# Performance work log

Hardware: AMD Instinct MI355X
Metric: run time of the kernel (lower is better)

## Reference

```python
import jax, jax.numpy as jnp
import numpy as np

N, M, NNZ, N_C, D = 4096, 4096, 262144, 4, 128
ADD_RATIO, TEMP = 0.1, 0.5


def setup_inputs() -> dict:
    key = jax.random.key(0)
    ks = jax.random.split(key, 6)
    X = jax.random.normal(ks[0], (N, D), dtype=jnp.float32)
    V = jax.random.randint(ks[1], (NNZ,), 0, N)
    E = jax.random.randint(ks[2], (NNZ,), 0, M)
    # incidence matrix consistent with the (V, E) pairs
    H = jnp.zeros((N, M), jnp.float32).at[V, E].set(1.0)
    incident_mask_prob = jax.random.uniform(ks[3], (N, M), jnp.float32, 1e-4, 1.0 - 1e-4)
    cos_weight = jax.random.normal(ks[4], (N_C, D), dtype=jnp.float32)
    eps = jax.random.uniform(ks[5], (N, M), jnp.float32, 1e-6, 1.0 - 1e-6)
    return {"X": X, "H": H, "V": V, "E": E,
            "incident_mask_prob": incident_mask_prob,
            "cos_weight": cos_weight, "eps": eps}


def _l2norm(x):
    # F.normalize(p=2, dim=-1): x / max(||x||, 1e-12)
    return x / jnp.maximum(jnp.linalg.norm(x, axis=-1, keepdims=True), 1e-12)


def reference(X, H, V, E, incident_mask_prob, cos_weight, eps):
    # scatter-mean of node embeddings into edge embeddings: eX [M, D]
    counts = jax.ops.segment_sum(jnp.ones((NNZ,), X.dtype), E, num_segments=M)
    eX = jax.ops.segment_sum(X[V], E, num_segments=M) / jnp.maximum(counts, 1.0)[:, None]

    node_fc = _l2norm(X[:, None, :] * cos_weight[None])   # [N, C, D]
    edge_fc = _l2norm(eX[:, None, :] * cos_weight[None])  # [M, C, D]
    # mean over C of per-channel cosine sims -> S [N, M]
    S = jnp.einsum('ncd,mcd->nm', node_fc, edge_fc) / N_C
    S = S.at[V, E].set(-1e30)  # mask existing incidences

    num_add = max(1, int(ADD_RATIO * NNZ))
    _, idx = jax.lax.top_k(S.reshape(-1), num_add)
    row = idx // M
    col = idx % M
    delta_H = jnp.zeros_like(H).at[row, col].set(1.0)
    enriched_H = H + delta_H

    # gumbel-sigmoid with straight-through estimator
    logit = (jnp.log(eps) - jnp.log(1.0 - eps)
             + jnp.log(incident_mask_prob + 1e-8)
             - jnp.log(1.0 - incident_mask_prob + 1e-8))
    soft = jax.nn.sigmoid(logit / TEMP)
    hard = (soft > 0.5).astype(soft.dtype)
    incident_mask = hard - jax.lax.stop_gradient(soft) + soft
    return enriched_H * incident_mask
```

## Files before the change

### kernel.cpp

```cpp
#include <hip/hip_runtime.h>

#define N_NODES 4096
#define M_EDGES 4096
#define NNZ_K   262144
#define NCH     4
#define DIM     128
#define KDIM    512
#define NM      (N_NODES * M_EDGES)
#define NUM_ADD 26214
#define NCB     2048
#define NFB     32768
#define NSEG    8
#define SEGSTR  16
#define CAPSEG  32768
#define CAPSEG2 16384

#define EXD_OFF   0ull
#define AFC_OFF   4194304ull
#define BFC_OFF   8388608ull
#define BKT_OFF   12582912ull
#define CVAL_OFF  13631488ull
#define CIDX_OFF  15728640ull
#define CNT_OFF   17039360ull
#define OFFS_OFF  17055744ull
#define CUR_OFF   17072132ull
#define HIST_OFF  17088516ull
#define FHIST_OFF 17096708ull
#define SCL_OFF   17227784ull
#define SEGC_OFF  17227848ull
#define ZERO_BYTES (17228872ull - CNT_OFF)
#define NINV_OFF  17228928ull
#define EINV_OFF  17360000ull
#define CIDX2_OFF 17491072ull

typedef short bf16x8 __attribute__((ext_vector_type(8)));
typedef float f32x4  __attribute__((ext_vector_type(4)));

#define GLOAD_LDS16(gsrc, ldst)                                                 \
    __builtin_amdgcn_global_load_lds(                                           \
        (const __attribute__((address_space(1))) void*)(gsrc),                  \
        (__attribute__((address_space(3))) void*)(ldst), 16, 0, 0)

__device__ __forceinline__ int bin_c(float s) {
    int b = (int)floorf((s + 1.0f) * 1024.0f);
    return min(max(b, 0), NCB - 1);
}

__device__ __forceinline__ int fbin_of(double v, int bstar) {
    double lo = (double)(bstar - 12) * (2.0 / 2048.0) - 1.0;
    double wd = (28.0 * (2.0 / 2048.0)) / (double)NFB;
    int f = (int)floor((v - lo) / wd);
    return min(max(f, 0), NFB - 1);
}

__device__ __forceinline__ float hard_mask(float p, float e) {
    float logit = logf(e) - logf(1.0f - e) + logf(p + 1e-8f) - logf(1.0f - p + 1e-8f);
    float soft  = 1.0f / (1.0f + expf(-2.0f * logit));
    return (soft > 0.5f) ? 1.0f : 0.0f;
}

__device__ __forceinline__ unsigned short to_bf16_rtne(float f) {
    unsigned int b = __float_as_uint(f);
    b += 0x7FFFu + ((b >> 16) & 1u);
    return (unsigned short)(b >> 16);
}

__global__ void k_count(const int* __restrict__ E, int* __restrict__ cnt) {
    int k = blockIdx.x * 256 + threadIdx.x;
    if (k < NNZ_K) atomicAdd(&cnt[E[k]], 1);
}

__global__ __launch_bounds__(256) void k_scan(const int* __restrict__ cnt, int* __restrict__ offs) {
    __shared__ int part[256];
    int t = threadIdx.x;
    int loc[16]; int s = 0;
    for (int j = 0; j < 16; ++j) { loc[j] = cnt[t * 16 + j]; s += loc[j]; }
    part[t] = s;
    __syncthreads();
    if (t == 0) { int acc = 0; for (int i = 0; i < 256; ++i) { int v = part[i]; part[i] = acc; acc += v; } }
    __syncthreads();
    int acc = part[t];
    for (int j = 0; j < 16; ++j) { offs[t * 16 + j] = acc; acc += loc[j]; }
    if (t == 255) offs[4096] = acc;
}

__global__ void k_fill(const int* __restrict__ E, const int* __restrict__ offs,
                       int* __restrict__ cur, int* __restrict__ bkt) {
    int k = blockIdx.x * 256 + threadIdx.x;
    if (k < NNZ_K) {
        int e = E[k];
        int pos = atomicAdd(&cur[e], 1);
        bkt[offs[e] + pos] = k;
    }
}

__global__ __launch_bounds__(128) void k_edge_mean(
        const int* __restrict__ Vv, const int* __restrict__ cnt,
        const int* __restrict__ offs, const int* __restrict__ bkt,
        const float* __restrict__ X, double* __restrict__ eXd) {
    __shared__ int sk[1024];
    __shared__ int sv[1024];
    int m = blockIdx.x;
    int c = cnt[m]; if (c > 1024) c = 1024;
    int off = offs[m];
    for (int t = threadIdx.x; t < c; t += 128) sk[t] = bkt[off + t];
    __syncthreads();
    for (int t = threadIdx.x; t < c; t += 128) {
        int key = sk[t]; int r = 0;
        for (int j = 0; j < c; ++j) r += (sk[j] < key);
        sv[r] = Vv[key];
    }
    __syncthreads();
    int d = threadIdx.x;
    double s = 0.0;
    for (int j = 0; j < c; ++j) s += (double)X[sv[j] * DIM + d];
    eXd[m * DIM + d] = s / (double)(c > 1 ? c : 1);
}

template <typename T>
__global__ __launch_bounds__(128) void k_fc(const T* __restrict__ in,
                                            const float* __restrict__ w,
                                            unsigned short* __restrict__ out,
                                            double* __restrict__ dinv) {
    __shared__ double red[128];
    int n = blockIdx.x, d = threadIdx.x;
    double x = (double)in[n * DIM + d];
    for (int c = 0; c < NCH; ++c) {
        double v = x * (double)w[c * DIM + d];
        red[d] = v * v;
        __syncthreads();
        for (int s = 64; s > 0; s >>= 1) { if (d < s) red[d] += red[d + s]; __syncthreads(); }
        double denom = fmax(sqrt(red[0]), 1e-12);
        __syncthreads();
        out[n * KDIM + c * DIM + d] = to_bf16_rtne((float)(v / denom));
        if (d == 0) dinv[n * NCH + c] = 1.0 / denom;
    }
}

__global__ __launch_bounds__(256) void k_gemm_mfma(const unsigned short* __restrict__ A,
                                                   const unsigned short* __restrict__ B,
                                                   float* __restrict__ S) {
    __shared__ short As[128][32];
    __shared__ short Bs[128][32];
    int tid = threadIdx.x;
    int row0 = blockIdx.y * 128, col0 = blockIdx.x * 128;
    int w = tid >> 6, l = tid & 63;
    int wr = (w >> 1) * 64, wc = (w & 1) * 64;
    f32x4 acc[4][4] = {};
    int lrow = l >> 2, lcol = (l & 3) * 8;
    int rb0 = (w * 2 + 0) * 16, rb1 = (w * 2 + 1) * 16;
    const unsigned short* sA0 = A + (size_t)(row0 + rb0 + lrow) * KDIM + lcol;
    const unsigned short* sA1 = A + (size_t)(row0 + rb1 + lrow) * KDIM + lcol;
    const unsigned short* sB0 = B + (size_t)(col0 + rb0 + lrow) * KDIM + lcol;
    const unsigned short* sB1 = B + (size_t)(col0 + rb1 + lrow) * KDIM + lcol;
    for (int k0 = 0; k0 < KDIM; k0 += 32) {
        __syncthreads();
        GLOAD_LDS16(sA0 + k0, &As[rb0][0]);
        GLOAD_LDS16(sA1 + k0, &As[rb1][0]);
        GLOAD_LDS16(sB0 + k0, &Bs[rb0][0]);
        GLOAD_LDS16(sB1 + k0, &Bs[rb1][0]);
        __syncthreads();
        int kq = (l >> 4) * 8;
        bf16x8 af[4], bfr[4];
        #pragma unroll
        for (int m = 0; m < 4; ++m) af[m] = *(const bf16x8*)&As[wr + m * 16 + (l & 15)][kq];
        #pragma unroll
        for (int n = 0; n < 4; ++n) bfr[n] = *(const bf16x8*)&Bs[wc + n * 16 + (l & 15)][kq];
        #pragma unroll
        for (int m = 0; m < 4; ++m)
            #pragma unroll
            for (int n = 0; n < 4; ++n)
                acc[m][n] = __builtin_amdgcn_mfma_f32_16x16x32_bf16(af[m], bfr[n], acc[m][n], 0, 0, 0);
    }
    #pragma unroll
    for (int m = 0; m < 4; ++m) {
        int r = row0 + wr + m * 16 + (l >> 4) * 4;
        #pragma unroll
        for (int n = 0; n < 4; ++n) {
            int c = col0 + wc + n * 16 + (l & 15);
            #pragma unroll
            for (int j = 0; j < 4; ++j)
                S[(size_t)(r + j) * M_EDGES + c] = 0.25f * acc[m][n][j];
        }
    }
}

__global__ void k_mask(const int* __restrict__ Vv, const int* __restrict__ E,
                       float* __restrict__ S) {
    int k = blockIdx.x * 256 + threadIdx.x;
    if (k < NNZ_K) S[(size_t)Vv[k] * M_EDGES + E[k]] = -1e30f;
}

__global__ __launch_bounds__(256) void k_hist_coarse(const float4* __restrict__ S4,
                                                     int* __restrict__ hist) {
    __shared__ int h[4][NCB + 8];
    int t = threadIdx.x;
    for (int i = t; i < 4 * (NCB + 8); i += 256) ((int*)h)[i] = 0;
    __syncthreads();
    int* hc = h[t & 3];
    int stride = gridDim.x * 256;
    for (int i = blockIdx.x * 256 + t; i < NM / 4; i += stride) {
        float4 v = S4[i];
        if (v.x > -2.0f) atomicAdd(&hc[bin_c(v.x)], 1);
        if (v.y > -2.0f) atomicAdd(&hc[bin_c(v.y)], 1);
        if (v.z > -2.0f) atomicAdd(&hc[bin_c(v.z)], 1);
        if (v.w > -2.0f) atomicAdd(&hc[bin_c(v.w)], 1);
    }
    __syncthreads();
    for (int i = t; i < NCB; i += 256) {
        int s = h[0][i] + h[1][i] + h[2][i] + h[3][i];
        if (s) atomicAdd(&hist[i], s);
    }
}

__global__ __launch_bounds__(256) void k_findcut(const int* __restrict__ hist, int* __restrict__ scl) {
    __shared__ int part[256];
    __shared__ int sb;
    int t = threadIdx.x;
    int loc[8]; int s = 0;
    for (int j = 0; j < 8; ++j) { loc[j] = hist[t * 8 + j]; s += loc[j]; }
    part[t] = s;
    __syncthreads();
    if (t == 0) { int acc = 0; for (int i = 255; i >= 0; --i) { int v = part[i]; part[i] = acc; acc += v; } }
    __syncthreads();
    int run = part[t];
    for (int j = 7; j >= 0; --j) {
        int h = loc[j];
        run += h;
        if (run >= NUM_ADD && run - h < NUM_ADD) { scl[0] = t * 8 + j; sb = t * 8 + j; }
    }
    __syncthreads();
    int bstar = sb;
    int g = 0;
    for (int i = bstar + 11 + t; i < NCB; i += 256) g += hist[i];
    part[t] = g;
    __syncthreads();
    for (int st2 = 128; st2 > 0; st2 >>= 1) { if (t < st2) part[t] += part[t + st2]; __syncthreads(); }
    if (t == 0) scl[1] = part[0];
}

__global__ __launch_bounds__(256) void k_collect(float4* __restrict__ S4,
        const int* __restrict__ scl, unsigned long long* __restrict__ segc,
        int* __restrict__ cidx, int* __restrict__ cidx2) {
    __shared__ unsigned short buf1[4096];
    __shared__ unsigned short buf2[4096];
    __shared__ int c1, c2;
    __shared__ unsigned long long gbase;
    int t = threadIdx.x;
    if (t == 0) { c1 = 0; c2 = 0; }
    __syncthreads();
    int bstar = scl[0];
    size_t base4 = (size_t)blockIdx.x * 1024 + t;
    float4 v0 = S4[base4];
    float4 v1 = S4[base4 + 256];
    float4 v2 = S4[base4 + 512];
    float4 v3 = S4[base4 + 768];
    #define COLLECT1(sc, loc)                                                   \
        if ((sc) > -2.0f) {                                                     \
            int b = bin_c(sc);                                                  \
            if (b >= bstar + 11)      buf2[atomicAdd(&c2, 1)] = (unsigned short)(loc); \
            else if (b >= bstar - 11) buf1[atomicAdd(&c1, 1)] = (unsigned short)(loc); \
        }
    #define COLLECT4(v, q)                                                      \
        COLLECT1((v).x, (t + (q)*256) * 4 + 0) COLLECT1((v).y, (t + (q)*256) * 4 + 1) \
        COLLECT1((v).z, (t + (q)*256) * 4 + 2) COLLECT1((v).w, (t + (q)*256) * 4 + 3)
    COLLECT4(v0, 0) COLLECT4(v1, 1) COLLECT4(v2, 2) COLLECT4(v3, 3)
    #undef COLLECT4
    #undef COLLECT1
    float4 z = make_float4(0.f, 0.f, 0.f, 0.f);
    S4[base4] = z; S4[base4 + 256] = z; S4[base4 + 512] = z; S4[base4 + 768] = z;
    __syncthreads();
    int seg = blockIdx.x & (NSEG - 1);
    if (t == 0) {
        unsigned long long pack = (unsigned long long)(unsigned)c1
                                | ((unsigned long long)(unsigned)c2 << 32);
        gbase = atomicAdd(&segc[seg * SEGSTR], pack);
    }
    __syncthreads();
    int g1 = (int)(gbase & 0xffffffffull);
    int g2 = (int)(gbase >> 32);
    int gb = blockIdx.x * 4096;
    int* ci1 = cidx  + seg * CAPSEG;
    int* ci2 = cidx2 + seg * CAPSEG2;
    for (int j = t; j < c1; j += 256) { int g = g1 + j; if (g < CAPSEG)  ci1[g] = gb + buf1[j]; }
    for (int j = t; j < c2; j += 256) { int g = g2 + j; if (g < CAPSEG2) ci2[g] = gb + buf2[j]; }
}

__global__ void k_scatter(const int* __restrict__ Vv, const int* __restrict__ E,
                          const float* __restrict__ prob, const float* __restrict__ eps,
                          float* __restrict__ out) {
    int k = blockIdx.x * 256 + threadIdx.x;
    if (k < NNZ_K) {
        size_t idx = (size_t)Vv[k] * M_EDGES + E[k];
        out[idx] = hard_mask(prob[idx], eps[idx]);
    }
}

__global__ __launch_bounds__(256) void k_selc(const unsigned long long* __restrict__ segc,
        const int* __restrict__ cidx2,
        const float* __restrict__ prob, const float* __restrict__ eps,
        float* __restrict__ out) {
    for (int s = 0; s < NSEG; ++s) {
        int c2 = (int)(segc[s * SEGSTR] >> 32); if (c2 > CAPSEG2) c2 = CAPSEG2;
        const int* ci = cidx2 + s * CAPSEG2;
        for (int i = blockIdx.x * 256 + threadIdx.x; i < c2; i += 256 * 128) {
            int idx = ci[i];
            out[idx] = hard_mask(prob[idx], eps[idx]);
        }
    }
}

__global__ __launch_bounds__(256) void k_exact(
        const unsigned long long* __restrict__ segc, const int* __restrict__ cidx,
        double* __restrict__ cval,
        const float* __restrict__ X, const double* __restrict__ eXd, const float* __restrict__ cw,
        const double* __restrict__ ninv, const double* __restrict__ einv) {
    int wid = (blockIdx.x * 256 + threadIdx.x) >> 6;
    int l = threadIdx.x & 63;
    int nw = gridDim.x * 4;
    double w2[NCH][2];
    #pragma unroll
    for (int c = 0; c < NCH; ++c) {
        float2 wc2 = *(const float2*)&cw[c * DIM + 2 * l];
        w2[c][0] = (double)wc2.x * (double)wc2.x;
        w2[c][1] = (double)wc2.y * (double)wc2.y;
    }
    for (int s = 0; s < NSEG; ++s) {
        int nc = (int)(segc[s * SEGSTR] & 0xffffffffull); if (nc > CAPSEG) nc = CAPSEG;
        const int* ci = cidx + s * CAPSEG;
        double* cv = cval + s * CAPSEG;
        for (int i = wid; i < nc; i += nw) {
            int idx = ci[i];
            int n = idx >> 12, m = idx & (M_EDGES - 1);
            float2  x2 = *(const float2*)&X[n * DIM + 2 * l];
            double2 e2 = *(const double2*)&eXd[m * DIM + 2 * l];
            double p0 = (double)x2.x * e2.x;
            double p1 = (double)x2.y * e2.y;
            double dt0 = p0 * w2[0][0] + p1 * w2[0][1];
            double dt1 = p0 * w2[1][0] + p1 * w2[1][1];
            double dt2 = p0 * w2[2][0] + p1 * w2[2][1];
            double dt3 = p0 * w2[3][0] + p1 * w2[3][1];
            #pragma unroll
            for (int sh = 1; sh < 64; sh <<= 1) {
                dt0 += __shfl_xor(dt0, sh);
                dt1 += __shfl_xor(dt1, sh);
                dt2 += __shfl_xor(dt2, sh);
                dt3 += __shfl_xor(dt3, sh);
            }
            if (l == 0) {
                const double* nv = &ninv[n * NCH];
                const double* ev = &einv[m * NCH];
                cv[i] = 0.25 * (dt0 * nv[0] * ev[0] + dt1 * nv[1] * ev[1]
                              + dt2 * nv[2] * ev[2] + dt3 * nv[3] * ev[3]);
            }
        }
    }
}

__global__ __launch_bounds__(256) void k_fhist(const unsigned long long* __restrict__ segc,
                                               const double* __restrict__ cval,
                                               const int* __restrict__ scl,
                                               int* __restrict__ fh) {
    int bstar = scl[0];
    for (int s = 0; s < NSEG; ++s) {
        int nc = (int)(segc[s * SEGSTR] & 0xffffffffull); if (nc > CAPSEG) nc = CAPSEG;
        const double* cv = cval + s * CAPSEG;
        for (int i = blockIdx.x * 256 + threadIdx.x; i < nc; i += 256 * 256)
            atomicAdd(&fh[fbin_of(cv[i], bstar)], 1);
    }
}

__global__ __launch_bounds__(1024) void k_ffind(const int* __restrict__ fh, int* __restrict__ scl) {
    __shared__ int part[1024];
    int T = NUM_ADD - scl[1];
    int t = threadIdx.x;
    int loc[32]; int s = 0;
    for (int j = 0; j < 32; ++j) { loc[j] = fh[t * 32 + j]; s += loc[j]; }
    part[t] = s;
    __syncthreads();
    if (t == 0) { int acc = 0; for (int i = 1023; i >= 0; --i) { int v = part[i]; part[i] = acc; acc += v; } }
    __syncthreads();
    int run = part[t];
    for (int j = 31; j >= 0; --j) {
        int h = loc[j];
        run += h;
        if (run >= T && run - h < T) { scl[4] = t * 32 + j; scl[5] = run - h; }
    }
}

__global__ __launch_bounds__(256) void k_write(
        const unsigned long long* __restrict__ segc, const int* __restrict__ cidx,
        const double* __restrict__ cval, const int* __restrict__ scl,
        const float* __restrict__ prob, const float* __restrict__ eps,
        float* __restrict__ out) {
    int fs = scl[4], bstar = scl[0];
    for (int s = 0; s < NSEG; ++s) {
        int nc = (int)(segc[s * SEGSTR] & 0xffffffffull); if (nc > CAPSEG) nc = CAPSEG;
        const int* ci = cidx + s * CAPSEG;
        const double* cv = cval + s * CAPSEG;
        for (int i = blockIdx.x * 256 + threadIdx.x; i < nc; i += 256 * 256) {
            if (fbin_of(cv[i], bstar) > fs) {
                int idx = ci[i];
                out[idx] = hard_mask(prob[idx], eps[idx]);
            }
        }
    }
}

__global__ __launch_bounds__(256) void k_tie(
        const unsigned long long* __restrict__ segc, const int* __restrict__ cidx,
        const double* __restrict__ cval, const int* __restrict__ scl,
        const float* __restrict__ prob, const float* __restrict__ eps,
        float* __restrict__ out) {
    __shared__ double mv[256];
    __shared__ int    mi[256];
    __shared__ int    cnt;
    int T = NUM_ADD - scl[1];
    int fs = scl[4], G1f = scl[5], bstar = scl[0];
    int t = threadIdx.x;
    if (t == 0) cnt = 0;
    __syncthreads();
    for (int s = 0; s < NSEG; ++s) {
        int nc = (int)(segc[s * SEGSTR] & 0xffffffffull); if (nc > CAPSEG) nc = CAPSEG;
        const double* cv = cval + s * CAPSEG;
        const int* ci = cidx + s * CAPSEG;
        for (int i = t; i < nc; i += 256) {
            if (fbin_of(cv[i], bstar) == fs) {
                int sl = atomicAdd(&cnt, 1);
                if (sl < 256) { mv[sl] = cv[i]; mi[sl] = ci[i]; }
            }
        }
    }
    __syncthreads();
    int nm = min(cnt, 256);
    for (int k = t; k < nm; k += 256) {
        double v = mv[k]; int idx = mi[k];
        int rank = G1f;
        for (int j = 0; j < nm; ++j)
            rank += (mv[j] > v || (mv[j] == v && mi[j] < idx)) ? 1 : 0;
        if (rank < T)
            out[idx] = hard_mask(prob[idx], eps[idx]);
    }
}

extern "C" void kernel_launch(void* const* d_in, const int* in_sizes, int n_in,
                              void* d_out, int out_size, void* d_ws, size_t ws_size,
                              hipStream_t stream) {
    const float* X    = (const float*)d_in[0];
    const int*   Vv   = (const int*)d_in[2];
    const int*   E    = (const int*)d_in[3];
    const float* prob = (const float*)d_in[4];
    const float* cw   = (const float*)d_in[5];
    const float* eps  = (const float*)d_in[6];
    float* out = (float*)d_out;
    char*  ws  = (char*)d_ws;

    double*             eXd   = (double*)(ws + EXD_OFF);
    unsigned short*     Afc   = (unsigned short*)(ws + AFC_OFF);
    unsigned short*     Bfc   = (unsigned short*)(ws + BFC_OFF);
    int*                bkt   = (int*)(ws + BKT_OFF);
    double*             cval  = (double*)(ws + CVAL_OFF);
    int*                cidx  = (int*)(ws + CIDX_OFF);
    int*                cidx2 = (int*)(ws + CIDX2_OFF);
    int*                cnt   = (int*)(ws + CNT_OFF);
    int*                offs  = (int*)(ws + OFFS_OFF);
    int*                cur   = (int*)(ws + CUR_OFF);
    int*                hist  = (int*)(ws + HIST_OFF);
    int*                fh    = (int*)(ws + FHIST_OFF);
    int*                scl   = (int*)(ws + SCL_OFF);
    unsigned long long* segc  = (unsigned long long*)(ws + SEGC_OFF);
    double*             ninv  = (double*)(ws + NINV_OFF);
    double*             einv  = (double*)(ws + EINV_OFF);

    hipMemsetAsync(ws + CNT_OFF, 0, (size_t)ZERO_BYTES, stream);

    k_count<<<NNZ_K / 256, 256, 0, stream>>>(E, cnt);
    k_scan<<<1, 256, 0, stream>>>(cnt, offs);
    k_fill<<<NNZ_K / 256, 256, 0, stream>>>(E, offs, cur, bkt);
    k_edge_mean<<<M_EDGES, 128, 0, stream>>>(Vv, cnt, offs, bkt, X, eXd);
    k_fc<float><<<N_NODES, 128, 0, stream>>>(X, cw, Afc, ninv);
    k_fc<double><<<M_EDGES, 128, 0, stream>>>(eXd, cw, Bfc, einv);
    dim3 gg(M_EDGES / 128, N_NODES / 128);
    k_gemm_mfma<<<gg, 256, 0, stream>>>(Afc, Bfc, out);
    k_mask<<<NNZ_K / 256, 256, 0, stream>>>(Vv, E, out);
    k_hist_coarse<<<1024, 256, 0, stream>>>((const float4*)out, hist);
    k_findcut<<<1, 256, 0, stream>>>(hist, scl);
    k_collect<<<4096, 256, 0, stream>>>((float4*)out, scl, segc, cidx, cidx2);
    k_scatter<<<NNZ_K / 256, 256, 0, stream>>>(Vv, E, prob, eps, out);
    k_selc<<<128, 256, 0, stream>>>(segc, cidx2, prob, eps, out);
    k_exact<<<1024, 256, 0, stream>>>(segc, cidx, cval, X, eXd, cw, ninv, einv);
    k_fhist<<<256, 256, 0, stream>>>(segc, cval, scl, fh);
    k_ffind<<<1, 1024, 0, stream>>>(fh, scl);
    k_write<<<256, 256, 0, stream>>>(segc, cidx, cval, scl, prob, eps, out);
    k_tie<<<1, 256, 0, stream>>>(segc, cidx, cval, scl, prob, eps, out);
}
```

Before: 285.0 us.

## Double K-tile depth and XOR-swizzle LDS layout in MFMA GEMM

Raises the GEMM K-step from 32 to 64, halving the number of loop iterations and barrier pairs. It also applies an XOR swizzle to the column chunk positions in LDS so that the fragment reads spread across banks. The cost is twice the LDS per block and more fragment registers per iteration. Occupancy may drop, and the swizzle indexing has to match exactly between the writes and the reads.

After: 281.0 us. Within noise of the previous version (-1.4%).

```diff
diff --git a/kernel.cpp b/kernel.cpp
--- a/kernel.cpp
+++ b/kernel.cpp
@@ -140,37 +140,52 @@
 __global__ __launch_bounds__(256) void k_gemm_mfma(const unsigned short* __restrict__ A,
                                                    const unsigned short* __restrict__ B,
                                                    float* __restrict__ S) {
-    __shared__ short As[128][32];
-    __shared__ short Bs[128][32];
+    __shared__ short As[128][64];
+    __shared__ short Bs[128][64];
     int tid = threadIdx.x;
     int row0 = blockIdx.y * 128, col0 = blockIdx.x * 128;
     int w = tid >> 6, l = tid & 63;
     int wr = (w >> 1) * 64, wc = (w & 1) * 64;
     f32x4 acc[4][4] = {};
-    int lrow = l >> 2, lcol = (l & 3) * 8;
-    int rb0 = (w * 2 + 0) * 16, rb1 = (w * 2 + 1) * 16;
-    const unsigned short* sA0 = A + (size_t)(row0 + rb0 + lrow) * KDIM + lcol;
-    const unsigned short* sA1 = A + (size_t)(row0 + rb1 + lrow) * KDIM + lcol;
-    const unsigned short* sB0 = B + (size_t)(col0 + rb0 + lrow) * KDIM + lcol;
-    const unsigned short* sB1 = B + (size_t)(col0 + rb1 + lrow) * KDIM + lcol;
-    for (int k0 = 0; k0 < KDIM; k0 += 32) {
+    int srow = l >> 3;
+    int scol = ((l & 7) ^ srow) * 8;
+    int rbw = w * 32;
+    const unsigned short* gA[4];
+    const unsigned short* gB[4];
+    #pragma unroll
+    for (int i = 0; i < 4; ++i) {
+        gA[i] = A + (size_t)(row0 + rbw + i * 8 + srow) * KDIM + scol;
+        gB[i] = B + (size_t)(col0 + rbw + i * 8 + srow) * KDIM + scol;
+    }
+    int q = l >> 4;
+    int kq0 = ((q ^ (l & 7)) & 7) * 8;
+    int kq1 = (((4 + q) ^ (l & 7)) & 7) * 8;
+    for (int k0 = 0; k0 < KDIM; k0 += 64) {
         __syncthreads();
-        GLOAD_LDS16(sA0 + k0, &As[rb0][0]);
-        GLOAD_LDS16(sA1 + k0, &As[rb1][0]);
-        GLOAD_LDS16(sB0 + k0, &Bs[rb0][0]);
-        GLOAD_LDS16(sB1 + k0, &Bs[rb1][0]);
+        #pragma unroll
+        for (int i = 0; i < 4; ++i) {
+            GLOAD_LDS16(gA[i] + k0, &As[rbw + i * 8][0]);
+            GLOAD_LDS16(gB[i] + k0, &Bs[rbw + i * 8][0]);
+        }
         __syncthreads();
-        int kq = (l >> 4) * 8;
-        bf16x8 af[4], bfr[4];
+        bf16x8 af0[4], af1[4], bf0[4], bf1[4];
         #pragma unroll
-        for (int m = 0; m < 4; ++m) af[m] = *(const bf16x8*)&As[wr + m * 16 + (l & 15)][kq];
+        for (int m = 0; m < 4; ++m) {
+            af0[m] = *(const bf16x8*)&As[wr + m * 16 + (l & 15)][kq0];
+            af1[m] = *(const bf16x8*)&As[wr + m * 16 + (l & 15)][kq1];
+        }
         #pragma unroll
-        for (int n = 0; n < 4; ++n) bfr[n] = *(const bf16x8*)&Bs[wc + n * 16 + (l & 15)][kq];
+        for (int n = 0; n < 4; ++n) {
+            bf0[n] = *(const bf16x8*)&Bs[wc + n * 16 + (l & 15)][kq0];
+            bf1[n] = *(const bf16x8*)&Bs[wc + n * 16 + (l & 15)][kq1];
+        }
         #pragma unroll
         for (int m = 0; m < 4; ++m)
             #pragma unroll
-            for (int n = 0; n < 4; ++n)
-                acc[m][n] = __builtin_amdgcn_mfma_f32_16x16x32_bf16(af[m], bfr[n], acc[m][n], 0, 0, 0);
+            for (int n = 0; n < 4; ++n) {
+                acc[m][n] = __builtin_amdgcn_mfma_f32_16x16x32_bf16(af0[m], bf0[n], acc[m][n], 0, 0, 0);
+                acc[m][n] = __builtin_amdgcn_mfma_f32_16x16x32_bf16(af1[m], bf1[n], acc[m][n], 0, 0, 0);
+            }
     }
     #pragma unroll
     for (int m = 0; m < 4; ++m) {
```
